# Optimization experiments

Hardware: AMD Instinct MI355X
Metric: run time of the kernel (lower is better)

Reference implementation:

```python
import jax, jax.numpy as jnp
import numpy as np

N_HEAD = 8

def setup_inputs() -> dict:
    key = jax.random.key(0)
    ks = jax.random.split(key, 5)
    N, C, T, V = 64, 128, 64, 25
    x = jax.random.normal(ks[0], (N, C, T, V), dtype=jnp.float32)
    Wa = jax.random.normal(ks[1], (C, C), dtype=jnp.float32) * (1.0 / np.sqrt(C))
    ba = jax.random.normal(ks[2], (C,), dtype=jnp.float32) * 0.01
    Wp = jax.random.normal(ks[3], (C, C), dtype=jnp.float32) * (1.0 / np.sqrt(C))
    bp = jax.random.normal(ks[4], (C,), dtype=jnp.float32) * 0.01
    temp = jnp.ones((N_HEAD, 1), dtype=jnp.float32)
    denom_bias = jnp.zeros((N_HEAD, 1, 1), dtype=jnp.float32)
    return {"x": x, "Wa": Wa, "ba": ba, "Wp": Wp, "bp": bp, "temp": temp, "denom_bias": denom_bias}

def reference(x, Wa, ba, Wp, bp, temp, denom_bias):
    # x: (N, C, T, V); eval mode (dropout = identity); residual = identity (in==out, stride==1)
    N, C, T, V = x.shape
    H = N_HEAD
    hd = C // H
    res = x
    # 1x1 conv c_attn
    w = jnp.einsum('nctv,oc->notv', x, Wa) + ba[None, :, None, None]
    # (N,H,hd,T,V) -> (N,H,T,V,hd) -> (N,H,T*V,hd)
    w = w.reshape(N, H, hd, T, V).transpose(0, 1, 3, 4, 2).reshape(N, H, T * V, hd)
    w_sq = w * w
    denom = jnp.maximum(jnp.cumsum(w_sq, axis=2), 1e-12)
    w_normed = w_sq / denom + denom_bias  # denom_bias (H,1,1) broadcasts
    tmp = jnp.sum(w_normed, axis=-1) * temp  # (N,H,L) * (H,1)
    Pi = jax.nn.softmax(tmp, axis=2)  # (N,H,L)
    dots = jnp.cumsum(w_sq * Pi[..., None], axis=2) / (jnp.cumsum(Pi, axis=2) + 1e-8)[..., None]
    attn = 1.0 / (1.0 + dots)
    y = -(w * Pi[..., None]) * attn  # (N,H,L,hd)
    y = y.reshape(N, H, T, V, hd).transpose(0, 1, 4, 2, 3).reshape(N, C, T, V)
    y = jnp.einsum('nctv,oc->notv', y, Wp) + bp[None, :, None, None]
    y = y + res
    return jax.nn.relu(y)
```

## Files before the change

kernel.cpp:

```cpp
#include <hip/hip_runtime.h>
#include <hip/hip_bf16.h>

#define N_S     64
#define C_CH    128
#define L_SEQ   1600
#define H_HEADS 8
#define HD      16
#define SEG     50
#define PADW    136
#define PADT    72

typedef __attribute__((ext_vector_type(8))) short bf16x8;
typedef __attribute__((ext_vector_type(4))) float f32x4;

__device__ inline unsigned short f2bf(float f) {
  return __builtin_bit_cast(unsigned short, __float2bfloat16(f));
}
__device__ inline float bflo(unsigned int u) { return __builtin_bit_cast(float, u << 16); }
__device__ inline float bfhi(unsigned int u) { return __builtin_bit_cast(float, u & 0xffff0000u); }

__global__ __launch_bounds__(256) void k_gemm1(const float* __restrict__ x,
                                               const float* __restrict__ Wa,
                                               const float* __restrict__ ba,
                                               unsigned short* __restrict__ w2) {
  __shared__ unsigned short was[128 * PADW];
  __shared__ unsigned short xs[128 * PADT];
  const int n = blockIdx.y;
  const int l0 = blockIdx.x * 64;
  const int t = threadIdx.x;
  const float* xn = x + (size_t)n * (C_CH * L_SEQ);

#pragma unroll
  for (int it = 0; it < 16; ++it) {
    int pos = it * 256 + t;
    int o = pos >> 5;
    int c4 = (pos & 31) << 2;
    float4 v = *reinterpret_cast<const float4*>(Wa + o * C_CH + c4);
    ushort4 u;
    u.x = f2bf(v.x); u.y = f2bf(v.y); u.z = f2bf(v.z); u.w = f2bf(v.w);
    *reinterpret_cast<ushort4*>(&was[o * PADW + c4]) = u;
  }
#pragma unroll
  for (int it = 0; it < 8; ++it) {
    int pos = it * 256 + t;
    int c = pos >> 4;
    int l4 = (pos & 15) << 2;
    float4 v = *reinterpret_cast<const float4*>(xn + (size_t)c * L_SEQ + l0 + l4);
    ushort4 u;
    u.x = f2bf(v.x); u.y = f2bf(v.y); u.z = f2bf(v.z); u.w = f2bf(v.w);
    *reinterpret_cast<ushort4*>(&xs[c * PADT + l4]) = u;
  }
  __syncthreads();

  const int wv = t >> 6;
  const int lane = t & 63;
  const int r16 = lane & 15;
  const int kg = lane >> 4;
  f32x4 acc[8];
#pragma unroll
  for (int ot = 0; ot < 8; ++ot) acc[ot] = (f32x4){0.f, 0.f, 0.f, 0.f};

#pragma unroll
  for (int ks = 0; ks < 4; ++ks) {
    bf16x8 a;
#pragma unroll
    for (int j = 0; j < 8; ++j)
      a[j] = (short)xs[(ks * 32 + kg * 8 + j) * PADT + wv * 16 + r16];
#pragma unroll
    for (int ot = 0; ot < 8; ++ot) {
      bf16x8 b = *reinterpret_cast<const bf16x8*>(&was[(ot * 16 + r16) * PADW + ks * 32 + kg * 8]);
      acc[ot] = __builtin_amdgcn_mfma_f32_16x16x32_bf16(a, b, acc[ot], 0, 0, 0);
    }
  }
#pragma unroll
  for (int ot = 0; ot < 8; ++ot) {
    float bav = ba[ot * 16 + r16];
    ushort4 u;
    u.x = f2bf(acc[ot][0] + bav);
    u.y = f2bf(acc[ot][1] + bav);
    u.z = f2bf(acc[ot][2] + bav);
    u.w = f2bf(acc[ot][3] + bav);
    size_t idx = (((size_t)n * H_HEADS + ot) * HD + r16) * L_SEQ + l0 + wv * 16 + kg * 4;
    *reinterpret_cast<ushort4*>(&w2[idx]) = u;
  }
}

__global__ __launch_bounds__(512) void k_scan(const unsigned short* __restrict__ w2,
                                              unsigned short* __restrict__ y2,
                                              const float* __restrict__ temp,
                                              const float* __restrict__ dbias) {
  __shared__ float tmp_l[L_SEQ];
  __shared__ float cbuf[32][10][17];
  __shared__ float stot[32][17];
  __shared__ float pi_seg[32];
  __shared__ float red[16];
  const int nh = blockIdx.x;
  const int h = nh & 7;
  const int t = threadIdx.x;
  const int d = t & 15;
  const int seg = t >> 4;
  const int l0 = seg * SEG;
  const size_t base = ((size_t)nh * HD + d) * L_SEQ + l0;
  const float tscale = temp[h];
  const float db16 = 16.f * dbias[h];

  unsigned int vp[25];
#pragma unroll
  for (int ii = 0; ii < 25; ++ii)
    vp[ii] = *reinterpret_cast<const unsigned int*>(w2 + base + 2 * ii);

  float tot = 0.f;
#pragma unroll
  for (int ii = 0; ii < 25; ++ii) {
    float a = bflo(vp[ii]), b = bfhi(vp[ii]);
    tot += a * a + b * b;
  }
  stot[seg][d] = tot;
  __syncthreads();
  float off = 0.f;
#pragma unroll
  for (int s = 0; s < 32; ++s) { float q = stot[s][d]; if (s < seg) off += q; }

  {
    float run = off;
    const int s2 = t / 10;
    const int j2 = t - s2 * 10;
#pragma unroll
    for (int i0 = 0; i0 < SEG; i0 += 10) {
      float c0[10];
#pragma unroll
      for (int j = 0; j < 10; ++j) {
        int i = i0 + j;
        float v = (i & 1) ? bfhi(vp[i >> 1]) : bflo(vp[i >> 1]);
        float wsq = v * v;
        run += wsq;
        c0[j] = __fdividef(wsq, fmaxf(run, 1e-12f));
      }
      if (i0) __syncthreads();
#pragma unroll
      for (int j = 0; j < 10; ++j) cbuf[seg][j][d] = c0[j];
      __syncthreads();
      if (t < 320) {
        float a = 0.f;
#pragma unroll
        for (int dd = 0; dd < 16; ++dd) a += cbuf[s2][j2][dd];
        tmp_l[s2 * SEG + i0 + j2] = (a + db16) * tscale;
      }
    }
  }
  __syncthreads();

  float m = -3.0e38f;
  for (int l = t; l < L_SEQ; l += 512) m = fmaxf(m, tmp_l[l]);
#pragma unroll
  for (int mask = 32; mask; mask >>= 1) m = fmaxf(m, __shfl_xor(m, mask));
  const int wid = t >> 6;
  if ((t & 63) == 0) red[wid] = m;
  __syncthreads();
  float M = red[0];
#pragma unroll
  for (int i2 = 1; i2 < 8; ++i2) M = fmaxf(M, red[i2]);
  float s = 0.f;
  for (int l = t; l < L_SEQ; l += 512) {
    float e = __expf(tmp_l[l] - M);
    tmp_l[l] = e;
    s += e;
  }
#pragma unroll
  for (int mask = 32; mask; mask >>= 1) s += __shfl_xor(s, mask);
  if ((t & 63) == 0) red[8 + wid] = s;
  __syncthreads();
  float S = 0.f;
#pragma unroll
  for (int i2 = 0; i2 < 8; ++i2) S += red[8 + i2];
  const float ninvS = -1.0f / S;
  const float epsS = 1e-8f * S;

  float wp_tot = 0.f, pi_tot = 0.f;
#pragma unroll
  for (int ii = 0; ii < 25; ++ii) {
    float a = bflo(vp[ii]), b = bfhi(vp[ii]);
    float e0 = tmp_l[l0 + 2 * ii];
    float e1 = tmp_l[l0 + 2 * ii + 1];
    wp_tot += a * a * e0 + b * b * e1;
    pi_tot += e0 + e1;
  }
  stot[seg][d] = wp_tot;
  if (d == 0) pi_seg[seg] = pi_tot;
  __syncthreads();
  float wp_off = 0.f, pi_off = 0.f;
#pragma unroll
  for (int s2 = 0; s2 < 32; ++s2) {
    float vw = stot[s2][d];
    float vq = pi_seg[s2];
    if (s2 < seg) { wp_off += vw; pi_off += vq; }
  }

  {
    float run_wp = wp_off, run_pi = pi_off;
#pragma unroll
    for (int ii = 0; ii < 25; ++ii) {
      float v0 = bflo(vp[ii]), v1 = bfhi(vp[ii]);
      float e0 = tmp_l[l0 + 2 * ii];
      run_pi += e0;
      run_wp += v0 * v0 * e0;
      float dn0 = run_pi + epsS;
      float y0 = (v0 * e0) * __fdividef(dn0, dn0 + run_wp) * ninvS;
      float e1 = tmp_l[l0 + 2 * ii + 1];
      run_pi += e1;
      run_wp += v1 * v1 * e1;
      float dn1 = run_pi + epsS;
      float y1 = (v1 * e1) * __fdividef(dn1, dn1 + run_wp) * ninvS;
      vp[ii] = (unsigned int)f2bf(y0) | ((unsigned int)f2bf(y1) << 16);
    }
  }
#pragma unroll
  for (int ii = 0; ii < 25; ++ii)
    *reinterpret_cast<unsigned int*>(y2 + base + 2 * ii) = vp[ii];
}

__global__ __launch_bounds__(256) void k_gemm2(const unsigned short* __restrict__ y2,
                                               const float* __restrict__ Wp,
                                               const float* __restrict__ bp,
                                               const float* __restrict__ x,
                                               float* __restrict__ out) {
  __shared__ unsigned short wps[128 * PADW];
  __shared__ unsigned short ys[128 * PADT];
  const int n = blockIdx.y;
  const int l0 = blockIdx.x * 64;
  const int t = threadIdx.x;

#pragma unroll
  for (int it = 0; it < 16; ++it) {
    int pos = it * 256 + t;
    int o = pos >> 5;
    int c4 = (pos & 31) << 2;
    float4 v = *reinterpret_cast<const float4*>(Wp + o * C_CH + c4);
    ushort4 u;
    u.x = f2bf(v.x); u.y = f2bf(v.y); u.z = f2bf(v.z); u.w = f2bf(v.w);
    *reinterpret_cast<ushort4*>(&wps[o * PADW + c4]) = u;
  }
#pragma unroll
  for (int it = 0; it < 4; ++it) {
    int pos = it * 256 + t;
    int c = pos >> 3;
    int l8 = (pos & 7) << 3;
    uint4 v = *reinterpret_cast<const uint4*>(y2 + ((size_t)n * C_CH + c) * L_SEQ + l0 + l8);
    *reinterpret_cast<uint4*>(&ys[c * PADT + l8]) = v;
  }
  __syncthreads();

  const int wv = t >> 6;
  const int lane = t & 63;
  const int r16 = lane & 15;
  const int kg = lane >> 4;
  f32x4 acc[8];
#pragma unroll
  for (int ot = 0; ot < 8; ++ot) acc[ot] = (f32x4){0.f, 0.f, 0.f, 0.f};

#pragma unroll
  for (int ks = 0; ks < 4; ++ks) {
    bf16x8 b;
#pragma unroll
    for (int j = 0; j < 8; ++j)
      b[j] = (short)ys[(ks * 32 + kg * 8 + j) * PADT + wv * 16 + r16];
#pragma unroll
    for (int ot = 0; ot < 8; ++ot) {
      bf16x8 a = *reinterpret_cast<const bf16x8*>(&wps[(ot * 16 + r16) * PADW + ks * 32 + kg * 8]);
      acc[ot] = __builtin_amdgcn_mfma_f32_16x16x32_bf16(a, b, acc[ot], 0, 0, 0);
    }
  }
  const int gl = l0 + wv * 16 + r16;
#pragma unroll
  for (int ot = 0; ot < 8; ++ot) {
#pragma unroll
    for (int i = 0; i < 4; ++i) {
      int o = ot * 16 + kg * 4 + i;
      size_t idx = (size_t)n * (C_CH * L_SEQ) + (size_t)o * L_SEQ + gl;
      float r = acc[ot][i] + bp[o] + x[idx];
      out[idx] = fmaxf(r, 0.f);
    }
  }
}

extern "C" void kernel_launch(void* const* d_in, const int* in_sizes, int n_in,
                              void* d_out, int out_size, void* d_ws, size_t ws_size,
                              hipStream_t stream) {
  const float* x     = (const float*)d_in[0];
  const float* Wa    = (const float*)d_in[1];
  const float* ba    = (const float*)d_in[2];
  const float* Wp    = (const float*)d_in[3];
  const float* bp    = (const float*)d_in[4];
  const float* temp  = (const float*)d_in[5];
  const float* dbias = (const float*)d_in[6];
  float* out = (float*)d_out;

  unsigned short* w2 = (unsigned short*)d_ws;
  unsigned short* y2 = w2 + (size_t)N_S * H_HEADS * L_SEQ * HD;

  k_gemm1<<<dim3(L_SEQ / 64, N_S), 256, 0, stream>>>(x, Wa, ba, w2);
  k_scan<<<N_S * H_HEADS, 512, 0, stream>>>(w2, y2, temp, dbias);
  k_gemm2<<<dim3(L_SEQ / 64, N_S), 256, 0, stream>>>(y2, Wp, bp, x, out);
}
```

Baseline: 79.72 us.

## Use analytic softmax max bound and wave-local reductions in scan kernel

```diff
diff --git a/kernel.cpp b/kernel.cpp
--- a/kernel.cpp
+++ b/kernel.cpp
@@ -90,19 +90,24 @@
                                               const float* __restrict__ temp,
                                               const float* __restrict__ dbias) {
   __shared__ float tmp_l[L_SEQ];
-  __shared__ float cbuf[32][10][17];
+  __shared__ float cbufw[8 * 680];
   __shared__ float stot[32][17];
   __shared__ float pi_seg[32];
-  __shared__ float red[16];
+  __shared__ float red[8];
+
   const int nh = blockIdx.x;
   const int h = nh & 7;
   const int t = threadIdx.x;
   const int d = t & 15;
   const int seg = t >> 4;
+  const int wv = t >> 6;
+  const int lane = t & 63;
+  const int sl = lane >> 4;
   const int l0 = seg * SEG;
   const size_t base = ((size_t)nh * HD + d) * L_SEQ + l0;
   const float tscale = temp[h];
   const float db16 = 16.f * dbias[h];
+  const float M = fmaxf((16.f + db16) * tscale, db16 * tscale);
 
   unsigned int vp[25];
 #pragma unroll
@@ -121,58 +126,39 @@
 #pragma unroll
   for (int s = 0; s < 32; ++s) { float q = stot[s][d]; if (s < seg) off += q; }
 
-  {
-    float run = off;
-    const int s2 = t / 10;
-    const int j2 = t - s2 * 10;
-#pragma unroll
-    for (int i0 = 0; i0 < SEG; i0 += 10) {
-      float c0[10];
-#pragma unroll
-      for (int j = 0; j < 10; ++j) {
-        int i = i0 + j;
-        float v = (i & 1) ? bfhi(vp[i >> 1]) : bflo(vp[i >> 1]);
-        float wsq = v * v;
-        run += wsq;
-        c0[j] = __fdividef(wsq, fmaxf(run, 1e-12f));
-      }
-      if (i0) __syncthreads();
-#pragma unroll
-      for (int j = 0; j < 10; ++j) cbuf[seg][j][d] = c0[j];
-      __syncthreads();
-      if (t < 320) {
-        float a = 0.f;
-#pragma unroll
-        for (int dd = 0; dd < 16; ++dd) a += cbuf[s2][j2][dd];
-        tmp_l[s2 * SEG + i0 + j2] = (a + db16) * tscale;
-      }
-    }
-  }
-  __syncthreads();
-
-  float m = -3.0e38f;
-  for (int l = t; l < L_SEQ; l += 512) m = fmaxf(m, tmp_l[l]);
-#pragma unroll
-  for (int mask = 32; mask; mask >>= 1) m = fmaxf(m, __shfl_xor(m, mask));
-  const int wid = t >> 6;
-  if ((t & 63) == 0) red[wid] = m;
-  __syncthreads();
-  float M = red[0];
-#pragma unroll
-  for (int i2 = 1; i2 < 8; ++i2) M = fmaxf(M, red[i2]);
-  float s = 0.f;
-  for (int l = t; l < L_SEQ; l += 512) {
-    float e = __expf(tmp_l[l] - M);
-    tmp_l[l] = e;
-    s += e;
-  }
-#pragma unroll
-  for (int mask = 32; mask; mask >>= 1) s += __shfl_xor(s, mask);
-  if ((t & 63) == 0) red[8 + wid] = s;
+  float* cw = &cbufw[wv * 680];
+  const int rsl = lane / 10;
+  const int rj = lane - rsl * 10;
+  float run = off;
+  float sAcc = 0.f;
+#pragma unroll
+  for (int i0 = 0; i0 < SEG; i0 += 10) {
+#pragma unroll
+    for (int j = 0; j < 10; ++j) {
+      int i = i0 + j;
+      float v = (i & 1) ? bfhi(vp[i >> 1]) : bflo(vp[i >> 1]);
+      float wsq = v * v;
+      run += wsq;
+      cw[(sl * 10 + j) * 17 + d] = __fdividef(wsq, fmaxf(run, 1e-12f));
+    }
+    __builtin_amdgcn_wave_barrier();
+    if (lane < 40) {
+      float a = 0.f;
+#pragma unroll
+      for (int dd = 0; dd < 16; ++dd) a += cw[(rsl * 10 + rj) * 17 + dd];
+      float e = __expf((a + db16) * tscale - M);
+      tmp_l[(4 * wv + rsl) * SEG + i0 + rj] = e;
+      sAcc += e;
+    }
+    __builtin_amdgcn_wave_barrier();
+  }
+#pragma unroll
+  for (int mask = 32; mask; mask >>= 1) sAcc += __shfl_xor(sAcc, mask);
+  if (lane == 0) red[wv] = sAcc;
   __syncthreads();
   float S = 0.f;
 #pragma unroll
-  for (int i2 = 0; i2 < 8; ++i2) S += red[8 + i2];
+  for (int i2 = 0; i2 < 8; ++i2) S += red[i2];
   const float ninvS = -1.0f / S;
   const float epsS = 1e-8f * S;
 
```

After: 77.05 us. 3.3% less time.
